# Optimization experiments

Hardware: AMD Instinct MI355X
Metric: run time of the kernel (lower is better)

The kernel has to match this reference:

```python
import jax, jax.numpy as jnp
import numpy as np

B = 32768
T = 1024  # num_time_bins


def setup_inputs() -> dict:
    key = jax.random.key(0)
    k1, k2, k3, k4 = jax.random.split(key, 4)
    hazard_values = jax.random.uniform(k1, (B, T), dtype=jnp.float32)
    labels_Y = jax.random.uniform(k2, (B,), dtype=jnp.float32) * T
    # nn.Linear(T, T): weight [T, T] (out, in), bias [T]
    lim = 1.0 / np.sqrt(T)
    W = jax.random.uniform(k3, (T, T), minval=-lim, maxval=lim, dtype=jnp.float32)
    b = jax.random.uniform(k4, (T,), minval=-lim, maxval=lim, dtype=jnp.float32)
    return {"hazard_values": hazard_values, "labels_Y": labels_Y, "W": W, "b": b}


def reference(hazard_values, labels_Y, W, b):
    # linear + sigmoid + argmax -> per-row truncation position
    logits = hazard_values @ W.T + b                       # [B, T]
    trunc_pos = jnp.argmax(jax.nn.sigmoid(logits), axis=1, keepdims=True)  # [B, 1] int
    # survival curve
    S = jnp.cumprod(1.0 - hazard_values, axis=1)           # [B, T]
    # vectorized truncation decay: for t >= p, multiply by exp(-(t - p))
    t = jnp.arange(T)[None, :]                             # [1, T]
    decay = jnp.where(t >= trunc_pos,
                      jnp.exp(-(t - trunc_pos).astype(S.dtype)),
                      jnp.ones((), S.dtype))
    S = S * decay
    # MSE between argmax position and labels (original prints; we skip prints)
    p = trunc_pos[:, 0].astype(jnp.float32)
    truncation_loss = jnp.mean((p - labels_Y) ** 2)
    return trunc_pos, S, truncation_loss
```

## Files before the change

### kernel.cpp

```cpp
#include <hip/hip_runtime.h>

#define B_ROWS 32768
#define T_BINS 1024

typedef __attribute__((ext_vector_type(8))) _Float16 half8;
typedef __attribute__((ext_vector_type(4))) float floatx4;

__device__ __forceinline__ unsigned long long pack_max(float v, int col) {
    unsigned x = __float_as_uint(v);
    x = (x & 0x80000000u) ? ~x : (x | 0x80000000u);
    return ((unsigned long long)x << 32) | (unsigned)(~col);
}

__device__ __forceinline__ void async16h(const _Float16* g, _Float16* l) {
    __builtin_amdgcn_global_load_lds(
        (const __attribute__((address_space(1))) unsigned int*)g,
        (__attribute__((address_space(3))) unsigned int*)l,
        16, 0, 0);
}

__global__ __launch_bounds__(256) void tof16_kernel(
    const float* __restrict__ src, _Float16* __restrict__ dst, int n4)
{
    int idx = blockIdx.x * 256 + threadIdx.x;
    if (idx >= n4) return;
    float4 x = ((const float4*)src)[idx];
    union { _Float16 h[4]; ushort4 u; } cv;
    cv.h[0] = (_Float16)x.x;
    cv.h[1] = (_Float16)x.y;
    cv.h[2] = (_Float16)x.z;
    cv.h[3] = (_Float16)x.w;
    ((ushort4*)dst)[idx] = cv.u;
}

__global__ __launch_bounds__(256, 3) void mega_kernel(
    const float* __restrict__ A, const _Float16* __restrict__ Wh,
    const float* __restrict__ bias, const float* __restrict__ labels,
    float* __restrict__ out_trunc, float* __restrict__ out_S,
    float* __restrict__ loss_acc)
{
    __shared__ _Float16 sA[2][64 * 32];
    __shared__ _Float16 sW[2][256 * 32];
    __shared__ unsigned long long cand[4][64];
    __shared__ float trunc_s[64];

    const int tid  = threadIdx.x;
    const int lane = tid & 63;
    const int wc   = tid >> 6;
    const int by   = blockIdx.x;

    const int arow = tid >> 2;
    const int akg  = (tid & 3) * 8;
    const float* Abase = A + (size_t)(by * 64 + arow) * T_BINS + akg;
    const int sAoff = arow * 32 + akg;

    const int ko = (lane >> 4) * 8;

    float run_best[4][4];
    int   run_col[4][4];
#pragma unroll
    for (int i = 0; i < 4; ++i)
#pragma unroll
        for (int r = 0; r < 4; ++r) { run_best[i][r] = -3.4e38f; run_col[i][r] = 0; }

    {
        float4 f0 = *(const float4*)(Abase);
        float4 f1 = *(const float4*)(Abase + 4);
        half8 hv;
        hv[0] = (_Float16)f0.x; hv[1] = (_Float16)f0.y;
        hv[2] = (_Float16)f0.z; hv[3] = (_Float16)f0.w;
        hv[4] = (_Float16)f1.x; hv[5] = (_Float16)f1.y;
        hv[6] = (_Float16)f1.z; hv[7] = (_Float16)f1.w;
        *(half8*)&sA[0][sAoff] = hv;
    }
#pragma unroll
    for (int r = 0; r < 4; ++r) {
        int c = r * 256 + tid;
        int wrow = c >> 2, wkc = (c & 3) * 8;
        async16h(Wh + (size_t)wrow * T_BINS + wkc, &sW[0][(r * 256 + wc * 64) * 8]);
    }
    float4 pa0 = *(const float4*)(Abase + 32);
    float4 pa1 = *(const float4*)(Abase + 36);
    __syncthreads();

    int n = 0;
    for (int bx = 0; bx < 4; ++bx) {
        const int colbase = bx * 256 + wc * 64 + (lane & 15);
        float bj[4];
#pragma unroll
        for (int j = 0; j < 4; ++j) bj[j] = bias[colbase + j * 16];

        floatx4 acc[4][4];
#pragma unroll
        for (int i = 0; i < 4; ++i)
#pragma unroll
            for (int j = 0; j < 4; ++j) acc[i][j] = (floatx4){0.f, 0.f, 0.f, 0.f};

        for (int t = 0; t < 32; ++t, ++n) {
            const int cur = n & 1;
            const int nxt = cur ^ 1;
            const int m   = (n + 1) & 127;
            const int bxn = m >> 5;
            const int k0n = (m & 31) * 32;

            const int kq = ((n + 2) & 31) * 32;
            float4 qa0 = *(const float4*)(Abase + kq);
            float4 qa1 = *(const float4*)(Abase + kq + 4);

#pragma unroll
            for (int r = 0; r < 4; ++r) {
                int c = r * 256 + tid;
                int wrow = c >> 2, wkc = (c & 3) * 8;
                async16h(Wh + (size_t)(bxn * 256 + wrow) * T_BINS + k0n + wkc,
                         &sW[nxt][(r * 256 + wc * 64) * 8]);
            }

            {
                half8 hv;
                hv[0] = (_Float16)pa0.x; hv[1] = (_Float16)pa0.y;
                hv[2] = (_Float16)pa0.z; hv[3] = (_Float16)pa0.w;
                hv[4] = (_Float16)pa1.x; hv[5] = (_Float16)pa1.y;
                hv[6] = (_Float16)pa1.z; hv[7] = (_Float16)pa1.w;
                *(half8*)&sA[nxt][sAoff] = hv;
            }
            pa0 = qa0; pa1 = qa1;

            half8 ah[4], whf[4];
#pragma unroll
            for (int i = 0; i < 4; ++i)
                ah[i] = *(const half8*)&sA[cur][(i * 16 + (lane & 15)) * 32 + ko];
#pragma unroll
            for (int j = 0; j < 4; ++j)
                whf[j] = *(const half8*)&sW[cur][(wc * 64 + j * 16 + (lane & 15)) * 32 + ko];
#pragma unroll
            for (int i = 0; i < 4; ++i)
#pragma unroll
                for (int j = 0; j < 4; ++j)
                    acc[i][j] = __builtin_amdgcn_mfma_f32_16x16x32_f16(ah[i], whf[j], acc[i][j], 0, 0, 0);

            __syncthreads();
        }

#pragma unroll
        for (int i = 0; i < 4; ++i)
#pragma unroll
            for (int r = 0; r < 4; ++r)
#pragma unroll
                for (int j = 0; j < 4; ++j) {
                    float v = acc[i][j][r] + bj[j];
                    if (v > run_best[i][r]) { run_best[i][r] = v; run_col[i][r] = colbase + j * 16; }
                }
    }

#pragma unroll
    for (int i = 0; i < 4; ++i)
#pragma unroll
        for (int r = 0; r < 4; ++r) {
            float best = run_best[i][r];
            int   bc   = run_col[i][r];
#pragma unroll
            for (int off = 8; off >= 1; off >>= 1) {
                float ov = __shfl_xor(best, off, 64);
                int   oc = __shfl_xor(bc, off, 64);
                if (ov > best || (ov == best && oc < bc)) { best = ov; bc = oc; }
            }
            if ((lane & 15) == 0)
                cand[wc][i * 16 + (lane >> 4) * 4 + r] = pack_max(best, bc);
        }
    __syncthreads();

    if (tid < 64) {
        unsigned long long m01 = cand[0][tid] > cand[1][tid] ? cand[0][tid] : cand[1][tid];
        unsigned long long m23 = cand[2][tid] > cand[3][tid] ? cand[2][tid] : cand[3][tid];
        unsigned long long mm = m01 > m23 ? m01 : m23;
        unsigned col = ~(unsigned)mm;
        float p = (float)col;
        int rowG = by * 64 + tid;
        out_trunc[rowG] = p;
        trunc_s[tid] = p;
        float d = p - labels[rowG];
        float term = d * d * (1.0f / (float)B_ROWS);
#pragma unroll
        for (int off = 32; off >= 1; off >>= 1)
            term += __shfl_down(term, off, 64);
        if (tid == 0) atomicAdd(loss_acc, term);
    }
    __syncthreads();

    for (int rr = 0; rr < 16; ++rr) {
        int row  = wc * 16 + rr;
        int rowG = by * 64 + row;
        const float* Hrow = A + (size_t)rowG * T_BINS + lane * 16;
        float4 h0 = *(const float4*)(Hrow + 0);
        float4 h1 = *(const float4*)(Hrow + 4);
        float4 h2 = *(const float4*)(Hrow + 8);
        float4 h3 = *(const float4*)(Hrow + 12);
        float hv[16] = {h0.x, h0.y, h0.z, h0.w, h1.x, h1.y, h1.z, h1.w,
                        h2.x, h2.y, h2.z, h2.w, h3.x, h3.y, h3.z, h3.w};
        float vprod[16];
        float run = 1.f;
#pragma unroll
        for (int j = 0; j < 16; ++j) { run *= (1.f - hv[j]); vprod[j] = run; }
        float x = run;
#pragma unroll
        for (int off = 1; off < 64; off <<= 1) {
            float o = __shfl_up(x, off, 64);
            if (lane >= off) x *= o;
        }
        float pre = __shfl_up(x, 1, 64);
        if (lane == 0) pre = 1.f;

        int p  = (int)trunc_s[row];
        int t0 = lane * 16;
        float sv[16];
#pragma unroll
        for (int j = 0; j < 16; ++j) {
            float s = pre * vprod[j];
            int t = t0 + j;
            if (t >= p) s *= __expf((float)(p - t));
            sv[j] = s;
        }
        float* Srow = out_S + (size_t)rowG * T_BINS + lane * 16;
        *(float4*)(Srow + 0)  = (float4){sv[0],  sv[1],  sv[2],  sv[3]};
        *(float4*)(Srow + 4)  = (float4){sv[4],  sv[5],  sv[6],  sv[7]};
        *(float4*)(Srow + 8)  = (float4){sv[8],  sv[9],  sv[10], sv[11]};
        *(float4*)(Srow + 12) = (float4){sv[12], sv[13], sv[14], sv[15]};
    }
}

#define BMf 64
#define BKf 16
#define LDSS (BMf + 4)
__global__ __launch_bounds__(256) void gemm_argmax_fp32(
    const float* __restrict__ A, const float* __restrict__ W,
    const float* __restrict__ bias, unsigned long long* __restrict__ rec)
{
    __shared__ float As[BKf][LDSS];
    __shared__ float Ws[BKf][LDSS];
    const int tid = threadIdx.x;
    const int tx = tid & 15, ty = tid >> 4;
    const int bx = blockIdx.x, by = blockIdx.y;
    const int ar = tid >> 2, ak = (tid & 3) << 2;
    const float* Arow = A + (size_t)(by * BMf + ar) * T_BINS + ak;
    const float* Wrow = W + (size_t)(bx * BMf + ar) * T_BINS + ak;
    float acc[4][4];
#pragma unroll
    for (int i = 0; i < 4; ++i)
#pragma unroll
        for (int j = 0; j < 4; ++j) acc[i][j] = 0.f;
    for (int k0 = 0; k0 < T_BINS; k0 += BKf) {
        float4 av = *(const float4*)(Arow + k0);
        float4 wvv = *(const float4*)(Wrow + k0);
        As[ak + 0][ar] = av.x; As[ak + 1][ar] = av.y; As[ak + 2][ar] = av.z; As[ak + 3][ar] = av.w;
        Ws[ak + 0][ar] = wvv.x; Ws[ak + 1][ar] = wvv.y; Ws[ak + 2][ar] = wvv.z; Ws[ak + 3][ar] = wvv.w;
        __syncthreads();
#pragma unroll
        for (int k = 0; k < BKf; ++k) {
            float4 a4 = *(const float4*)&As[k][ty * 4];
            float4 w4 = *(const float4*)&Ws[k][tx * 4];
            float aa[4] = {a4.x, a4.y, a4.z, a4.w};
            float ww[4] = {w4.x, w4.y, w4.z, w4.w};
#pragma unroll
            for (int i = 0; i < 4; ++i)
#pragma unroll
                for (int j = 0; j < 4; ++j) acc[i][j] = fmaf(aa[i], ww[j], acc[i][j]);
        }
        __syncthreads();
    }
    const int colBase = bx * BMf + tx * 4;
    float bv[4];
#pragma unroll
    for (int j = 0; j < 4; ++j) bv[j] = bias[colBase + j];
#pragma unroll
    for (int i = 0; i < 4; ++i) {
        float best = acc[i][0] + bv[0];
        int bc = colBase;
#pragma unroll
        for (int j = 1; j < 4; ++j) {
            float v = acc[i][j] + bv[j];
            if (v > best) { best = v; bc = colBase + j; }
        }
#pragma unroll
        for (int off = 8; off >= 1; off >>= 1) {
            float ov = __shfl_xor(best, off, 64);
            int oc = __shfl_xor(bc, off, 64);
            if (ov > best || (ov == best && oc < bc)) { best = ov; bc = oc; }
        }
        if (tx == 0) atomicMax(&rec[by * BMf + ty * 4 + i], pack_max(best, bc));
    }
}

__global__ __launch_bounds__(256) void finalize_kernel(
    const unsigned long long* __restrict__ rec, const float* __restrict__ labels,
    float* __restrict__ out_trunc, float* __restrict__ loss_acc)
{
    int i = blockIdx.x * 256 + threadIdx.x;
    unsigned col = ~(unsigned)(rec[i] & 0xFFFFFFFFull);
    float p = (float)col;
    out_trunc[i] = p;
    float d = p - labels[i];
    float term = d * d * (1.0f / (float)B_ROWS);
#pragma unroll
    for (int off = 32; off >= 1; off >>= 1)
        term += __shfl_down(term, off, 64);
    __shared__ float partials[4];
    int lane = threadIdx.x & 63, wv = threadIdx.x >> 6;
    if (lane == 0) partials[wv] = term;
    __syncthreads();
    if (threadIdx.x == 0)
        atomicAdd(loss_acc, partials[0] + partials[1] + partials[2] + partials[3]);
}

__global__ __launch_bounds__(256) void scan_kernel_f32(
    const float* __restrict__ H, const float* __restrict__ trunc_f,
    float* __restrict__ Sout)
{
    const int row = blockIdx.x;
    const int tid = threadIdx.x;
    const int lane = tid & 63;
    const int wv = tid >> 6;
    const float4 h = *(const float4*)(H + (size_t)row * T_BINS + tid * 4);
    float l0 = 1.f - h.x;
    float l1 = l0 * (1.f - h.y);
    float l2 = l1 * (1.f - h.z);
    float l3 = l2 * (1.f - h.w);
    float x = l3;
#pragma unroll
    for (int off = 1; off < 64; off <<= 1) {
        float o = __shfl_up(x, off, 64);
        if (lane >= off) x *= o;
    }
    float ex = __shfl_up(x, 1, 64);
    if (lane == 0) ex = 1.f;
    __shared__ float wtot[4];
    if (lane == 63) wtot[wv] = x;
    __syncthreads();
    float wpre = 1.f;
#pragma unroll
    for (int w = 0; w < 3; ++w)
        if (w < wv) wpre *= wtot[w];
    float pre = wpre * ex;
    int p = (int)trunc_f[row];
    int t0 = tid * 4;
    float sv[4] = {pre * l0, pre * l1, pre * l2, pre * l3};
#pragma unroll
    for (int j = 0; j < 4; ++j) {
        int t = t0 + j;
        if (t >= p) sv[j] *= __expf((float)(p - t));
    }
    float4 s4 = {sv[0], sv[1], sv[2], sv[3]};
    *(float4*)(Sout + (size_t)row * T_BINS + tid * 4) = s4;
}

extern "C" void kernel_launch(void* const* d_in, const int* in_sizes, int n_in,
                              void* d_out, int out_size, void* d_ws, size_t ws_size,
                              hipStream_t stream)
{
    const float* hazard = (const float*)d_in[0];
    const float* labels = (const float*)d_in[1];
    const float* W      = (const float*)d_in[2];
    const float* bias   = (const float*)d_in[3];

    float* out       = (float*)d_out;
    float* out_trunc = out;
    float* out_S     = out + B_ROWS;
    float* out_loss  = out + B_ROWS + (size_t)B_ROWS * T_BINS;

    hipMemsetAsync(out_loss, 0, sizeof(float), stream);

    const size_t NW = (size_t)T_BINS * T_BINS;
    if (ws_size >= NW * sizeof(_Float16)) {
        _Float16* Wh = (_Float16*)d_ws;
        tof16_kernel<<<(int)(NW / 4 / 256), 256, 0, stream>>>(W, Wh, (int)(NW / 4));
        mega_kernel<<<B_ROWS / 64, 256, 0, stream>>>(
            hazard, Wh, bias, labels, out_trunc, out_S, out_loss);
    } else {
        unsigned long long* rec = (unsigned long long*)out_S;
        hipMemsetAsync(rec, 0, (size_t)B_ROWS * sizeof(unsigned long long), stream);
        dim3 ggrid(T_BINS / BMf, B_ROWS / BMf);
        gemm_argmax_fp32<<<ggrid, 256, 0, stream>>>(hazard, W, bias, rec);
        finalize_kernel<<<B_ROWS / 256, 256, 0, stream>>>(rec, labels, out_trunc, out_loss);
        scan_kernel_f32<<<B_ROWS, 256, 0, stream>>>(hazard, out_trunc, out_S);
    }
}
```

Before: 380.4 us.

## Swizzle LDS tiles, replace syncthreads with fine waitcnt barriers, nontemporal S stores

XOR-swizzles the k-slot placement of the A and W fp16 tiles in shared memory so the MFMA operand reads avoid bank conflicts, and remaps the async global-to-LDS W loads to match. Full __syncthreads calls become explicit waitcnt plus s_barrier, allowing up to six outstanding vector-memory ops while the LDS reads are issued. Raises wave priority around the MFMA block and writes the survival output with nontemporal stores to keep it from polluting cache. The hand-tuned vmcnt depth depends on instruction ordering, so a miscount could cause a race on the async W tile.

Result: slower. 422.2 us (+11.0%).

```diff
diff --git a/kernel.cpp b/kernel.cpp
--- a/kernel.cpp
+++ b/kernel.cpp
@@ -49,12 +49,18 @@
     const int wc   = tid >> 6;
     const int by   = blockIdx.x;
 
-    const int arow = tid >> 2;
-    const int akg  = (tid & 3) * 8;
-    const float* Abase = A + (size_t)(by * 64 + arow) * T_BINS + akg;
-    const int sAoff = arow * 32 + akg;
-
-    const int ko = (lane >> 4) * 8;
+    const int arow  = tid >> 2;
+    const int aslot = tid & 3;
+    const int sAw   = arow * 32 + ((aslot ^ ((arow ^ (arow >> 2)) & 3)) * 8);
+    const float* Abase = A + (size_t)(by * 64 + arow) * T_BINS + aslot * 8;
+
+    const int l2    = lane >> 2;
+    const int wksw  = ((lane & 3) ^ ((l2 ^ (l2 >> 2)) & 3)) * 8;
+    const int wcol0 = wc * 64 + l2;
+
+    const int l15   = lane & 15;
+    const int hi    = lane >> 4;
+    const int rslot = ((hi ^ ((l15 ^ (l15 >> 2)) & 3)) * 8);
 
     float run_best[4][4];
     int   run_col[4][4];
@@ -71,21 +77,20 @@
         hv[2] = (_Float16)f0.z; hv[3] = (_Float16)f0.w;
         hv[4] = (_Float16)f1.x; hv[5] = (_Float16)f1.y;
         hv[6] = (_Float16)f1.z; hv[7] = (_Float16)f1.w;
-        *(half8*)&sA[0][sAoff] = hv;
-    }
-#pragma unroll
-    for (int r = 0; r < 4; ++r) {
-        int c = r * 256 + tid;
-        int wrow = c >> 2, wkc = (c & 3) * 8;
-        async16h(Wh + (size_t)wrow * T_BINS + wkc, &sW[0][(r * 256 + wc * 64) * 8]);
-    }
+        *(half8*)&sA[0][sAw] = hv;
+    }
+#pragma unroll
+    for (int r = 0; r < 4; ++r)
+        async16h(Wh + (size_t)(wcol0 + r * 16) * T_BINS + wksw,
+                 &sW[0][wc * 2048 + r * 512]);
     float4 pa0 = *(const float4*)(Abase + 32);
     float4 pa1 = *(const float4*)(Abase + 36);
-    __syncthreads();
+    asm volatile("s_waitcnt lgkmcnt(0)" ::: "memory");
+    __builtin_amdgcn_s_barrier();
 
     int n = 0;
     for (int bx = 0; bx < 4; ++bx) {
-        const int colbase = bx * 256 + wc * 64 + (lane & 15);
+        const int colbase = bx * 256 + wc * 64 + l15;
         float bj[4];
 #pragma unroll
         for (int j = 0; j < 4; ++j) bj[j] = bias[colbase + j * 16];
@@ -108,12 +113,9 @@
             float4 qa1 = *(const float4*)(Abase + kq + 4);
 
 #pragma unroll
-            for (int r = 0; r < 4; ++r) {
-                int c = r * 256 + tid;
-                int wrow = c >> 2, wkc = (c & 3) * 8;
-                async16h(Wh + (size_t)(bxn * 256 + wrow) * T_BINS + k0n + wkc,
-                         &sW[nxt][(r * 256 + wc * 64) * 8]);
-            }
+            for (int r = 0; r < 4; ++r)
+                async16h(Wh + (size_t)(bxn * 256 + wcol0 + r * 16) * T_BINS + k0n + wksw,
+                         &sW[nxt][wc * 2048 + r * 512]);
 
             {
                 half8 hv;
@@ -121,24 +123,30 @@
                 hv[2] = (_Float16)pa0.z; hv[3] = (_Float16)pa0.w;
                 hv[4] = (_Float16)pa1.x; hv[5] = (_Float16)pa1.y;
                 hv[6] = (_Float16)pa1.z; hv[7] = (_Float16)pa1.w;
-                *(half8*)&sA[nxt][sAoff] = hv;
+                *(half8*)&sA[nxt][sAw] = hv;
             }
             pa0 = qa0; pa1 = qa1;
 
+            asm volatile("s_waitcnt vmcnt(6)" ::: "memory");
+
             half8 ah[4], whf[4];
 #pragma unroll
             for (int i = 0; i < 4; ++i)
-                ah[i] = *(const half8*)&sA[cur][(i * 16 + (lane & 15)) * 32 + ko];
+                ah[i] = *(const half8*)&sA[cur][(i * 16 + l15) * 32 + rslot];
 #pragma unroll
             for (int j = 0; j < 4; ++j)
-                whf[j] = *(const half8*)&sW[cur][(wc * 64 + j * 16 + (lane & 15)) * 32 + ko];
+                whf[j] = *(const half8*)&sW[cur][(wc * 64 + j * 16 + l15) * 32 + rslot];
+
+            __builtin_amdgcn_s_setprio(1);
 #pragma unroll
             for (int i = 0; i < 4; ++i)
 #pragma unroll
                 for (int j = 0; j < 4; ++j)
                     acc[i][j] = __builtin_amdgcn_mfma_f32_16x16x32_f16(ah[i], whf[j], acc[i][j], 0, 0, 0);
-
-            __syncthreads();
+            __builtin_amdgcn_s_setprio(0);
+
+            asm volatile("s_waitcnt lgkmcnt(0)" ::: "memory");
+            __builtin_amdgcn_s_barrier();
         }
 
 #pragma unroll
@@ -220,11 +228,15 @@
             if (t >= p) s *= __expf((float)(p - t));
             sv[j] = s;
         }
-        float* Srow = out_S + (size_t)rowG * T_BINS + lane * 16;
-        *(float4*)(Srow + 0)  = (float4){sv[0],  sv[1],  sv[2],  sv[3]};
-        *(float4*)(Srow + 4)  = (float4){sv[4],  sv[5],  sv[6],  sv[7]};
-        *(float4*)(Srow + 8)  = (float4){sv[8],  sv[9],  sv[10], sv[11]};
-        *(float4*)(Srow + 12) = (float4){sv[12], sv[13], sv[14], sv[15]};
+        floatx4* Srow = (floatx4*)(out_S + (size_t)rowG * T_BINS + lane * 16);
+        floatx4 s0 = {sv[0],  sv[1],  sv[2],  sv[3]};
+        floatx4 s1 = {sv[4],  sv[5],  sv[6],  sv[7]};
+        floatx4 s2 = {sv[8],  sv[9],  sv[10], sv[11]};
+        floatx4 s3 = {sv[12], sv[13], sv[14], sv[15]};
+        __builtin_nontemporal_store(s0, Srow + 0);
+        __builtin_nontemporal_store(s1, Srow + 1);
+        __builtin_nontemporal_store(s2, Srow + 2);
+        __builtin_nontemporal_store(s3, Srow + 3);
     }
 }
 
```

## Double K-tile depth to 64 with XOR-swizzled LDS layout

Applied to the files above, without the earlier changes.

The GEMM main loop now stages 64-wide K tiles instead of 32, which halves the number of barrier-separated iterations. A and W tiles in LDS use an XOR swizzle to avoid bank conflicts on the wider rows. The cand/trunc_s scratch arrays are aliased onto sA to save LDS, and launch bounds drop to 2 blocks per CU because each block now needs more shared memory. Fewer syncs and fewer conflicts are traded against lower occupancy.

Measured after the change: 352.8 us. 7.3% less time.

```diff
diff --git a/kernel.cpp b/kernel.cpp
--- a/kernel.cpp
+++ b/kernel.cpp
@@ -33,16 +33,14 @@
     ((ushort4*)dst)[idx] = cv.u;
 }
 
-__global__ __launch_bounds__(256, 3) void mega_kernel(
+__global__ __launch_bounds__(256, 2) void mega_kernel(
     const float* __restrict__ A, const _Float16* __restrict__ Wh,
     const float* __restrict__ bias, const float* __restrict__ labels,
     float* __restrict__ out_trunc, float* __restrict__ out_S,
     float* __restrict__ loss_acc)
 {
-    __shared__ _Float16 sA[2][64 * 32];
-    __shared__ _Float16 sW[2][256 * 32];
-    __shared__ unsigned long long cand[4][64];
-    __shared__ float trunc_s[64];
+    __shared__ _Float16 sA[2][64 * 64];
+    __shared__ _Float16 sW[2][256 * 64];
 
     const int tid  = threadIdx.x;
     const int lane = tid & 63;
@@ -50,11 +48,18 @@
     const int by   = blockIdx.x;
 
     const int arow = tid >> 2;
-    const int akg  = (tid & 3) * 8;
-    const float* Abase = A + (size_t)(by * 64 + arow) * T_BINS + akg;
-    const int sAoff = arow * 32 + akg;
-
-    const int ko = (lane >> 4) * 8;
+    const int ac   = tid & 3;
+    const int x8a  = (arow ^ (arow >> 3)) & 7;
+    const int sAw0 = arow * 64 + (((ac * 2) ^ x8a) * 8);
+    const int sAw1 = arow * 64 + (((ac * 2 + 1) ^ x8a) * 8);
+    const float* Abase = A + (size_t)(by * 64 + arow) * T_BINS + ac * 16;
+
+    const int l3   = lane >> 3;
+    const int wsl  = lane & 7;
+
+    const int l15  = lane & 15;
+    const int hi   = lane >> 4;
+    const int xc   = (l15 & 7) ^ (l15 >> 3);
 
     float run_best[4][4];
     int   run_col[4][4];
@@ -64,28 +69,31 @@
         for (int r = 0; r < 4; ++r) { run_best[i][r] = -3.4e38f; run_col[i][r] = 0; }
 
     {
-        float4 f0 = *(const float4*)(Abase);
+        float4 f0 = *(const float4*)(Abase + 0);
         float4 f1 = *(const float4*)(Abase + 4);
-        half8 hv;
-        hv[0] = (_Float16)f0.x; hv[1] = (_Float16)f0.y;
-        hv[2] = (_Float16)f0.z; hv[3] = (_Float16)f0.w;
-        hv[4] = (_Float16)f1.x; hv[5] = (_Float16)f1.y;
-        hv[6] = (_Float16)f1.z; hv[7] = (_Float16)f1.w;
-        *(half8*)&sA[0][sAoff] = hv;
-    }
-#pragma unroll
-    for (int r = 0; r < 4; ++r) {
-        int c = r * 256 + tid;
-        int wrow = c >> 2, wkc = (c & 3) * 8;
-        async16h(Wh + (size_t)wrow * T_BINS + wkc, &sW[0][(r * 256 + wc * 64) * 8]);
-    }
-    float4 pa0 = *(const float4*)(Abase + 32);
-    float4 pa1 = *(const float4*)(Abase + 36);
+        float4 f2 = *(const float4*)(Abase + 8);
+        float4 f3 = *(const float4*)(Abase + 12);
+        half8 h0, h1;
+        h0[0] = (_Float16)f0.x; h0[1] = (_Float16)f0.y; h0[2] = (_Float16)f0.z; h0[3] = (_Float16)f0.w;
+        h0[4] = (_Float16)f1.x; h0[5] = (_Float16)f1.y; h0[6] = (_Float16)f1.z; h0[7] = (_Float16)f1.w;
+        h1[0] = (_Float16)f2.x; h1[1] = (_Float16)f2.y; h1[2] = (_Float16)f2.z; h1[3] = (_Float16)f2.w;
+        h1[4] = (_Float16)f3.x; h1[5] = (_Float16)f3.y; h1[6] = (_Float16)f3.z; h1[7] = (_Float16)f3.w;
+        *(half8*)&sA[0][sAw0] = h0;
+        *(half8*)&sA[0][sAw1] = h1;
+    }
+#pragma unroll
+    for (int r = 0; r < 8; ++r)
+        async16h(Wh + (size_t)(wc * 64 + r * 8 + l3) * T_BINS + ((wsl ^ l3 ^ r) * 8),
+                 &sW[0][(wc * 64 + r * 8) * 64]);
+    float4 pa0 = *(const float4*)(Abase + 64);
+    float4 pa1 = *(const float4*)(Abase + 68);
+    float4 pa2 = *(const float4*)(Abase + 72);
+    float4 pa3 = *(const float4*)(Abase + 76);
     __syncthreads();
 
     int n = 0;
     for (int bx = 0; bx < 4; ++bx) {
-        const int colbase = bx * 256 + wc * 64 + (lane & 15);
+        const int colbase = bx * 256 + wc * 64 + l15;
         float bj[4];
 #pragma unroll
         for (int j = 0; j < 4; ++j) bj[j] = bias[colbase + j * 16];
@@ -96,47 +104,53 @@
 #pragma unroll
             for (int j = 0; j < 4; ++j) acc[i][j] = (floatx4){0.f, 0.f, 0.f, 0.f};
 
-        for (int t = 0; t < 32; ++t, ++n) {
+        for (int t = 0; t < 16; ++t, ++n) {
             const int cur = n & 1;
             const int nxt = cur ^ 1;
-            const int m   = (n + 1) & 127;
-            const int bxn = m >> 5;
-            const int k0n = (m & 31) * 32;
-
-            const int kq = ((n + 2) & 31) * 32;
-            float4 qa0 = *(const float4*)(Abase + kq);
+            const int m   = (n + 1) & 63;
+            const int bxn = m >> 4;
+            const int k0n = (m & 15) * 64;
+
+            const int kq = ((n + 2) & 15) * 64;
+            float4 qa0 = *(const float4*)(Abase + kq + 0);
             float4 qa1 = *(const float4*)(Abase + kq + 4);
-
-#pragma unroll
-            for (int r = 0; r < 4; ++r) {
-                int c = r * 256 + tid;
-                int wrow = c >> 2, wkc = (c & 3) * 8;
-                async16h(Wh + (size_t)(bxn * 256 + wrow) * T_BINS + k0n + wkc,
-                         &sW[nxt][(r * 256 + wc * 64) * 8]);
+            float4 qa2 = *(const float4*)(Abase + kq + 8);
+            float4 qa3 = *(const float4*)(Abase + kq + 12);
+
+#pragma unroll
+            for (int r = 0; r < 8; ++r)
+                async16h(Wh + (size_t)(bxn * 256 + wc * 64 + r * 8 + l3) * T_BINS
+                            + k0n + ((wsl ^ l3 ^ r) * 8),
+                         &sW[nxt][(wc * 64 + r * 8) * 64]);
+
+            {
+                half8 h0, h1;
+                h0[0] = (_Float16)pa0.x; h0[1] = (_Float16)pa0.y; h0[2] = (_Float16)pa0.z; h0[3] = (_Float16)pa0.w;
+                h0[4] = (_Float16)pa1.x; h0[5] = (_Float16)pa1.y; h0[6] = (_Float16)pa1.z; h0[7] = (_Float16)pa1.w;
+                h1[0] = (_Float16)pa2.x; h1[1] = (_Float16)pa2.y; h1[2] = (_Float16)pa2.z; h1[3] = (_Float16)pa2.w;
+                h1[4] = (_Float16)pa3.x; h1[5] = (_Float16)pa3.y; h1[6] = (_Float16)pa3.z; h1[7] = (_Float16)pa3.w;
+                *(half8*)&sA[nxt][sAw0] = h0;
+                *(half8*)&sA[nxt][sAw1] = h1;
             }
-
-            {
-                half8 hv;
-                hv[0] = (_Float16)pa0.x; hv[1] = (_Float16)pa0.y;
-                hv[2] = (_Float16)pa0.z; hv[3] = (_Float16)pa0.w;
-                hv[4] = (_Float16)pa1.x; hv[5] = (_Float16)pa1.y;
-                hv[6] = (_Float16)pa1.z; hv[7] = (_Float16)pa1.w;
-                *(half8*)&sA[nxt][sAoff] = hv;
+            pa0 = qa0; pa1 = qa1; pa2 = qa2; pa3 = qa3;
+
+#pragma unroll
+            for (int g = 0; g < 2; ++g) {
+                half8 ah[4], whf[4];
+#pragma unroll
+                for (int i = 0; i < 4; ++i)
+                    ah[i] = *(const half8*)&sA[cur][(i * 16 + l15) * 64
+                                                    + (((g * 4 + hi) ^ xc ^ (i * 2)) * 8)];
+#pragma unroll
+                for (int j = 0; j < 4; ++j)
+                    whf[j] = *(const half8*)&sW[cur][(wc * 64 + j * 16 + l15) * 64
+                                                     + (((g * 4 + hi) ^ xc ^ (j * 2)) * 8)];
+#pragma unroll
+                for (int i = 0; i < 4; ++i)
+#pragma unroll
+                    for (int j = 0; j < 4; ++j)
+                        acc[i][j] = __builtin_amdgcn_mfma_f32_16x16x32_f16(ah[i], whf[j], acc[i][j], 0, 0, 0);
             }
-            pa0 = qa0; pa1 = qa1;
-
-            half8 ah[4], whf[4];
-#pragma unroll
-            for (int i = 0; i < 4; ++i)
-                ah[i] = *(const half8*)&sA[cur][(i * 16 + (lane & 15)) * 32 + ko];
-#pragma unroll
-            for (int j = 0; j < 4; ++j)
-                whf[j] = *(const half8*)&sW[cur][(wc * 64 + j * 16 + (lane & 15)) * 32 + ko];
-#pragma unroll
-            for (int i = 0; i < 4; ++i)
-#pragma unroll
-                for (int j = 0; j < 4; ++j)
-                    acc[i][j] = __builtin_amdgcn_mfma_f32_16x16x32_f16(ah[i], whf[j], acc[i][j], 0, 0, 0);
 
             __syncthreads();
         }
@@ -151,6 +165,9 @@
                     if (v > run_best[i][r]) { run_best[i][r] = v; run_col[i][r] = colbase + j * 16; }
                 }
     }
+
+    unsigned long long (*cand)[64] = reinterpret_cast<unsigned long long (*)[64]>(&sA[0][0]);
+    float* trunc_s = reinterpret_cast<float*>(&sA[0][0]) + 512;
 
 #pragma unroll
     for (int i = 0; i < 4; ++i)
```
